# Kernel optimization log

Hardware: AMD Instinct MI355X
Metric: run time of the kernel (lower is better)

Reference implementation:

```python
import jax, jax.numpy as jnp
import numpy as np

B, S, D, H = 2, 2048, 1024, 16
DK = D // H


def setup_inputs() -> dict:
    key = jax.random.key(0)
    ks = jax.random.split(key, 11)
    scale = 1.0 / np.sqrt(D)
    inp = {
        "q": jax.random.normal(ks[0], (B, S, D), jnp.float32),
        "k": jax.random.normal(ks[1], (B, S, D), jnp.float32),
        "v": jax.random.normal(ks[2], (B, S, D), jnp.float32),
        # causal mask, broadcastable to (B, H, S, S); 0 = masked
        "mask": jnp.tril(jnp.ones((S, S), jnp.int32))[None, None, :, :],
        "wq": jax.random.normal(ks[3], (D, D), jnp.float32) * scale,
        "bq": jax.random.normal(ks[4], (D,), jnp.float32) * scale,
        "wk": jax.random.normal(ks[5], (D, D), jnp.float32) * scale,
        "bk": jax.random.normal(ks[6], (D,), jnp.float32) * scale,
        "wv": jax.random.normal(ks[7], (D, D), jnp.float32) * scale,
        "bv": jax.random.normal(ks[8], (D,), jnp.float32) * scale,
        "wo": jax.random.normal(ks[9], (D, D), jnp.float32) * scale,
        "bo": jax.random.normal(ks[10], (D,), jnp.float32) * scale,
    }
    return inp


def reference(q, k, v, mask, wq, bq, wk, bk, wv, bv, wo, bo):
    # Linear projections (torch Linear: y = x @ W^T + b)
    Q = jnp.einsum('bsd,ed->bse', q, wq) + bq
    K = jnp.einsum('bsd,ed->bse', k, wk) + bk
    V = jnp.einsum('bsd,ed->bse', v, wv) + bv
    # split heads -> (B, H, S, d_k)
    Q = Q.reshape(B, S, H, DK).transpose(0, 2, 1, 3)
    K = K.reshape(B, S, H, DK).transpose(0, 2, 1, 3)
    V = V.reshape(B, S, H, DK).transpose(0, 2, 1, 3)
    # naive full-score attention, faithful to the source
    scores = jnp.einsum('bhqd,bhkd->bhqk', Q, K) / jnp.sqrt(jnp.float32(DK))
    scores = jnp.where(mask == 0, -jnp.inf, scores)
    attn = jax.nn.softmax(scores, axis=-1)
    out = jnp.einsum('bhqk,bhkd->bhqd', attn, V)
    # merge heads -> (B, S, D)
    out = out.transpose(0, 2, 1, 3).reshape(B, S, D)
    return jnp.einsum('bsd,ed->bse', out, wo) + bo
```

## Files before the change

kernel.cpp:

```cpp
#include <hip/hip_runtime.h>
#include <hip/hip_bf16.h>
#include <cstdint>

constexpr int Bc = 2, Sc = 2048, Dc = 1024, Hc = 16;
constexpr int Mtok = Bc * Sc;

typedef __bf16 bf16;
typedef __bf16 bf16x8 __attribute__((ext_vector_type(8)));
typedef float  f32x4  __attribute__((ext_vector_type(4)));

__device__ __forceinline__ void gld_lds16(const bf16* g, bf16* l) {
  __builtin_amdgcn_global_load_lds(
      (__attribute__((address_space(1))) void*)(void*)g,
      (__attribute__((address_space(3))) void*)l, 16, 0, 0);
}

__global__ __launch_bounds__(256) void convert_all(
    const float* __restrict__ q, const float* __restrict__ k,
    const float* __restrict__ v, const float* __restrict__ wq,
    const float* __restrict__ wk, const float* __restrict__ wv,
    const float* __restrict__ wo, bf16* __restrict__ ws)
{
  constexpr size_t NQ = (size_t)Mtok * Dc;
  constexpr size_t NW = (size_t)Dc * Dc;
  const size_t e = ((size_t)blockIdx.x * 256 + threadIdx.x) * 8;
  const float* src; bf16* dst;
  if (e < 3 * NQ) {
    src = (e < NQ) ? q + e : (e < 2 * NQ) ? k + (e - NQ) : v + (e - 2 * NQ);
    dst = ws + e;
  } else {
    const size_t w = e - 3 * NQ;
    const float* wsrc = (w < NW) ? wq : (w < 2 * NW) ? wk : (w < 3 * NW) ? wv : wo;
    src = wsrc + (w & (NW - 1));
    dst = ws + 5 * NQ + w;
  }
  f32x4 a = ((const f32x4*)src)[0];
  f32x4 b = ((const f32x4*)src)[1];
  bf16x8 t;
  t[0]=(bf16)a[0]; t[1]=(bf16)a[1]; t[2]=(bf16)a[2]; t[3]=(bf16)a[3];
  t[4]=(bf16)b[0]; t[5]=(bf16)b[1]; t[6]=(bf16)b[2]; t[7]=(bf16)b[3];
  *(bf16x8*)dst = t;
}

__global__ __launch_bounds__(256) void gemm_qkv(
    const bf16* __restrict__ Aq, const bf16* __restrict__ Ak,
    const bf16* __restrict__ Av, const bf16* __restrict__ Wb,
    const float* __restrict__ bq, const float* __restrict__ bk,
    const float* __restrict__ bv,
    bf16* __restrict__ Yq, bf16* __restrict__ Yk, bf16* __restrict__ Yv)
{
  __shared__ __attribute__((aligned(16))) bf16 As[128 * 32];
  __shared__ __attribute__((aligned(16))) bf16 Bs[128 * 32];

  const int z = blockIdx.z;
  const bf16*  A    = (z == 0) ? Aq : (z == 1) ? Ak : Av;
  const bf16*  Wz   = Wb + (size_t)z * Dc * Dc;
  const float* bias = (z == 0) ? bq : (z == 1) ? bk : bv;
  bf16*        Y    = (z == 0) ? Yq : (z == 1) ? Yk : Yv;

  const int m0 = blockIdx.x * 128, n0 = blockIdx.y * 128;
  const int tid = threadIdx.x, wave = tid >> 6, lane = tid & 63;
  const int quad = lane >> 4, l16 = lane & 15;
  const int rw = wave >> 1, cw = wave & 1;
  const int srow = wave * 16 + (lane >> 2);
  const int scol = (lane & 3) * 8;

  f32x4 acc[4][4] = {};

  for (int k0 = 0; k0 < Dc; k0 += 32) {
#pragma unroll
    for (int s = 0; s < 2; ++s) {
      const int row = s * 64 + srow;
      gld_lds16(A  + (size_t)(m0 + row) * Dc + k0 + scol, &As[s * 2048 + wave * 512]);
      gld_lds16(Wz + (size_t)(n0 + row) * Dc + k0 + scol, &Bs[s * 2048 + wave * 512]);
    }
    __syncthreads();
    bf16x8 af[4];
#pragma unroll
    for (int rt = 0; rt < 4; ++rt)
      af[rt] = *(const bf16x8*)&As[(rw * 64 + rt * 16 + l16) * 32 + quad * 8];
#pragma unroll
    for (int ct = 0; ct < 4; ++ct) {
      bf16x8 bfr = *(const bf16x8*)&Bs[(cw * 64 + ct * 16 + l16) * 32 + quad * 8];
#pragma unroll
      for (int rt = 0; rt < 4; ++rt)
        acc[rt][ct] = __builtin_amdgcn_mfma_f32_16x16x32_bf16(af[rt], bfr, acc[rt][ct], 0, 0, 0);
    }
    __syncthreads();
  }

#pragma unroll
  for (int ct = 0; ct < 4; ++ct) {
    const int col = n0 + cw * 64 + ct * 16 + l16;
    const float bvv = bias[col];
#pragma unroll
    for (int rt = 0; rt < 4; ++rt)
#pragma unroll
      for (int i = 0; i < 4; ++i) {
        const int row = m0 + rw * 64 + rt * 16 + quad * 4 + i;
        Y[(size_t)row * Dc + col] = (bf16)(acc[rt][ct][i] + bvv);
      }
  }
}

__global__ __launch_bounds__(256) void gemm_o(
    const bf16* __restrict__ A, const bf16* __restrict__ Wz,
    const float* __restrict__ bias, float* __restrict__ Y)
{
  __shared__ __attribute__((aligned(16))) bf16 As[64 * 32];
  __shared__ __attribute__((aligned(16))) bf16 Bs[128 * 32];

  const int m0 = blockIdx.x * 64, n0 = blockIdx.y * 128;
  const int tid = threadIdx.x, wave = tid >> 6, lane = tid & 63;
  const int quad = lane >> 4, l16 = lane & 15;
  const int srow = wave * 16 + (lane >> 2);
  const int scol = (lane & 3) * 8;

  f32x4 acc[4][2] = {};

  for (int k0 = 0; k0 < Dc; k0 += 32) {
    gld_lds16(A + (size_t)(m0 + srow) * Dc + k0 + scol, &As[wave * 512]);
#pragma unroll
    for (int s = 0; s < 2; ++s) {
      const int row = s * 64 + srow;
      gld_lds16(Wz + (size_t)(n0 + row) * Dc + k0 + scol, &Bs[s * 2048 + wave * 512]);
    }
    __syncthreads();
    bf16x8 af[4];
#pragma unroll
    for (int rt = 0; rt < 4; ++rt)
      af[rt] = *(const bf16x8*)&As[(rt * 16 + l16) * 32 + quad * 8];
#pragma unroll
    for (int ct = 0; ct < 2; ++ct) {
      bf16x8 bfr = *(const bf16x8*)&Bs[(wave * 32 + ct * 16 + l16) * 32 + quad * 8];
#pragma unroll
      for (int rt = 0; rt < 4; ++rt)
        acc[rt][ct] = __builtin_amdgcn_mfma_f32_16x16x32_bf16(af[rt], bfr, acc[rt][ct], 0, 0, 0);
    }
    __syncthreads();
  }

#pragma unroll
  for (int ct = 0; ct < 2; ++ct) {
    const int col = n0 + wave * 32 + ct * 16 + l16;
    const float bvv = bias[col];
#pragma unroll
    for (int rt = 0; rt < 4; ++rt)
#pragma unroll
      for (int i = 0; i < 4; ++i) {
        const int row = m0 + rt * 16 + quad * 4 + i;
        Y[(size_t)row * Dc + col] = acc[rt][ct][i] + bvv;
      }
  }
}

template <bool AF32, bool BF32, bool OUTF32>
__global__ __launch_bounds__(256) void gemm128(
    const void* __restrict__ Av, const void* __restrict__ Bv,
    const float* __restrict__ bias, void* __restrict__ Yv,
    int M, int N, int K)
{
  __shared__ __attribute__((aligned(16))) bf16 As[2][128][40];
  __shared__ __attribute__((aligned(16))) bf16 Bs[2][128][40];

  const int m0 = blockIdx.x * 128, n0 = blockIdx.y * 128;
  const int tid = threadIdx.x, wave = tid >> 6, lane = tid & 63;
  const int quad = lane >> 4, l16 = lane & 15;
  const int rw = wave >> 1, cw = wave & 1;
  const int srow = tid >> 1, sc = (tid & 1) * 16;

  f32x4 acc[4][4] = {};

  auto load = [&](const void* P, bool f32, int r0, int k0, bf16x8& lo, bf16x8& hi) {
    if (f32) {
      const float* s = (const float*)P + (size_t)(r0 + srow) * K + k0 + sc;
      f32x4 a0 = ((const f32x4*)s)[0], a1 = ((const f32x4*)s)[1];
      f32x4 a2 = ((const f32x4*)s)[2], a3 = ((const f32x4*)s)[3];
      lo[0]=(bf16)a0[0]; lo[1]=(bf16)a0[1]; lo[2]=(bf16)a0[2]; lo[3]=(bf16)a0[3];
      lo[4]=(bf16)a1[0]; lo[5]=(bf16)a1[1]; lo[6]=(bf16)a1[2]; lo[7]=(bf16)a1[3];
      hi[0]=(bf16)a2[0]; hi[1]=(bf16)a2[1]; hi[2]=(bf16)a2[2]; hi[3]=(bf16)a2[3];
      hi[4]=(bf16)a3[0]; hi[5]=(bf16)a3[1]; hi[6]=(bf16)a3[2]; hi[7]=(bf16)a3[3];
    } else {
      const bf16* s = (const bf16*)P + (size_t)(r0 + srow) * K + k0 + sc;
      lo = ((const bf16x8*)s)[0]; hi = ((const bf16x8*)s)[1];
    }
  };

  bf16x8 alo, ahi, blo, bhi;
  load(Av, AF32, m0, 0, alo, ahi); load(Bv, BF32, n0, 0, blo, bhi);
  *(bf16x8*)&As[0][srow][sc] = alo; *(bf16x8*)&As[0][srow][sc + 8] = ahi;
  *(bf16x8*)&Bs[0][srow][sc] = blo; *(bf16x8*)&Bs[0][srow][sc + 8] = bhi;

  const int NIT = K >> 5;
  for (int it = 0; it < NIT; ++it) {
    __syncthreads();
    const int cur = it & 1;
    const bool pf = (it + 1) < NIT;
    if (pf) { load(Av, AF32, m0, (it+1)*32, alo, ahi); load(Bv, BF32, n0, (it+1)*32, blo, bhi); }

    bf16x8 af[4];
#pragma unroll
    for (int rt = 0; rt < 4; ++rt)
      af[rt] = *(const bf16x8*)&As[cur][rw * 64 + rt * 16 + l16][quad * 8];
#pragma unroll
    for (int ct = 0; ct < 4; ++ct) {
      bf16x8 bfr = *(const bf16x8*)&Bs[cur][cw * 64 + ct * 16 + l16][quad * 8];
#pragma unroll
      for (int rt = 0; rt < 4; ++rt)
        acc[rt][ct] = __builtin_amdgcn_mfma_f32_16x16x32_bf16(af[rt], bfr, acc[rt][ct], 0, 0, 0);
    }
    if (pf) {
      const int nxt = cur ^ 1;
      *(bf16x8*)&As[nxt][srow][sc] = alo; *(bf16x8*)&As[nxt][srow][sc + 8] = ahi;
      *(bf16x8*)&Bs[nxt][srow][sc] = blo; *(bf16x8*)&Bs[nxt][srow][sc + 8] = bhi;
    }
  }

#pragma unroll
  for (int ct = 0; ct < 4; ++ct) {
    const int col = n0 + cw * 64 + ct * 16 + l16;
    const float bvv = bias[col];
#pragma unroll
    for (int rt = 0; rt < 4; ++rt)
#pragma unroll
      for (int i = 0; i < 4; ++i) {
        const int row = m0 + rw * 64 + rt * 16 + quad * 4 + i;
        const float vv = acc[rt][ct][i] + bvv;
        if constexpr (OUTF32) ((float*)Yv)[(size_t)row * N + col] = vv;
        else                  ((bf16*)Yv)[(size_t)row * N + col] = (bf16)vv;
      }
  }
}

__global__ __launch_bounds__(256) void transpose_v(
    const bf16* __restrict__ in, bf16* __restrict__ out)
{
  __shared__ __attribute__((aligned(16))) bf16 tile[64][72];
  const int s0 = blockIdx.x * 64, d0 = blockIdx.y * 64, b = blockIdx.z;
  const int t = threadIdx.x, r = t >> 2, c = (t & 3) * 16;

  const bf16* src = in + (size_t)(b * Sc + s0 + r) * Dc + d0 + c;
  *(bf16x8*)&tile[r][c]     = ((const bf16x8*)src)[0];
  *(bf16x8*)&tile[r][c + 8] = ((const bf16x8*)src)[1];
  __syncthreads();

  bf16x8 t0, t1;
#pragma unroll
  for (int j = 0; j < 8; ++j) t0[j] = tile[c + j][r];
#pragma unroll
  for (int j = 0; j < 8; ++j) t1[j] = tile[c + 8 + j][r];
  bf16* dst = out + (size_t)(b * Dc + d0 + r) * Sc + s0 + c;
  ((bf16x8*)dst)[0] = t0;
  ((bf16x8*)dst)[1] = t1;
}

__global__ __launch_bounds__(512) void attn3(
    const bf16* __restrict__ Q, const bf16* __restrict__ K,
    const bf16* __restrict__ Vt, bf16* __restrict__ O)
{
  __shared__ __attribute__((aligned(16))) bf16 Ks[2][64][68];
  __shared__ __attribute__((aligned(16))) bf16 Vs[2][64][68];
  __shared__ __attribute__((aligned(16))) bf16 Ps[8][16][68];

  const int bh = blockIdx.x, b = bh >> 4, h = bh & 15;
  const int pr = blockIdx.y;
  const int tid = threadIdx.x, wave = tid >> 6, lane = tid & 63;
  const int quad = lane >> 4, l16 = lane & 15;
  const int sr = tid >> 3, sc8 = (tid & 7) * 8;

  const bf16 onec = (bf16)1.0f;
  const bf16x8 ones = {onec, onec, onec, onec, onec, onec, onec, onec};

  for (int half = 0; half < 2; ++half) {
    const int qt = half ? (15 - pr) : pr;
    const int q0 = qt * 128;
    const int nkb = 2 * (qt + 1);

    const bf16* qrow = Q + (size_t)(b * Sc + q0 + wave * 16 + l16) * Dc + h * 64 + quad * 8;
    const bf16x8 aq0 = *(const bf16x8*)qrow;
    const bf16x8 aq1 = *(const bf16x8*)(qrow + 32);

    f32x4 oacc[4] = {{0,0,0,0},{0,0,0,0},{0,0,0,0},{0,0,0,0}};
    f32x4 lacc = {0, 0, 0, 0};

    __syncthreads();
    *(bf16x8*)&Ks[0][sr][sc8] = *(const bf16x8*)(K  + (size_t)(b * Sc + sr) * Dc + h * 64 + sc8);
    *(bf16x8*)&Vs[0][sr][sc8] = *(const bf16x8*)(Vt + (size_t)(b * Dc + h * 64 + sr) * Sc + sc8);

    for (int kb = 0; kb < nkb; ++kb) {
      __syncthreads();
      const int cur = kb & 1;
      const bool pf = (kb + 1) < nkb;
      bf16x8 kp, vp;
      if (pf) {
        kp = *(const bf16x8*)(K  + (size_t)(b * Sc + (kb + 1) * 64 + sr) * Dc + h * 64 + sc8);
        vp = *(const bf16x8*)(Vt + (size_t)(b * Dc + h * 64 + sr) * Sc + (kb + 1) * 64 + sc8);
      }

      f32x4 s[4] = {{0,0,0,0},{0,0,0,0},{0,0,0,0},{0,0,0,0}};
#pragma unroll
      for (int d2 = 0; d2 < 2; ++d2) {
        const bf16x8 a = d2 ? aq1 : aq0;
#pragma unroll
        for (int ct = 0; ct < 4; ++ct) {
          bf16x8 bk = *(const bf16x8*)&Ks[cur][ct * 16 + l16][d2 * 32 + quad * 8];
          s[ct] = __builtin_amdgcn_mfma_f32_16x16x32_bf16(a, bk, s[ct], 0, 0, 0);
        }
      }

      if (kb >= nkb - 2) {
        const int row = q0 + wave * 16 + quad * 4;
#pragma unroll
        for (int ct = 0; ct < 4; ++ct) {
          const int col = kb * 64 + ct * 16 + l16;
#pragma unroll
          for (int i = 0; i < 4; ++i) {
            const float e = (col > row + i) ? 0.f : __expf(s[ct][i] * 0.125f);
            Ps[wave][quad * 4 + i][ct * 16 + l16] = (bf16)e;
          }
        }
      } else {
#pragma unroll
        for (int ct = 0; ct < 4; ++ct)
#pragma unroll
          for (int i = 0; i < 4; ++i)
            Ps[wave][quad * 4 + i][ct * 16 + l16] = (bf16)__expf(s[ct][i] * 0.125f);
      }

      const bf16x8 ap0 = *(const bf16x8*)&Ps[wave][l16][quad * 8];
      const bf16x8 ap1 = *(const bf16x8*)&Ps[wave][l16][32 + quad * 8];

      lacc = __builtin_amdgcn_mfma_f32_16x16x32_bf16(ap0, ones, lacc, 0, 0, 0);
      lacc = __builtin_amdgcn_mfma_f32_16x16x32_bf16(ap1, ones, lacc, 0, 0, 0);

#pragma unroll
      for (int d2 = 0; d2 < 2; ++d2) {
        const bf16x8 ap = d2 ? ap1 : ap0;
#pragma unroll
        for (int ct = 0; ct < 4; ++ct) {
          bf16x8 bv = *(const bf16x8*)&Vs[cur][ct * 16 + l16][d2 * 32 + quad * 8];
          oacc[ct] = __builtin_amdgcn_mfma_f32_16x16x32_bf16(ap, bv, oacc[ct], 0, 0, 0);
        }
      }

      if (pf) {
        const int nxt = cur ^ 1;
        *(bf16x8*)&Ks[nxt][sr][sc8] = kp;
        *(bf16x8*)&Vs[nxt][sr][sc8] = vp;
      }
    }

    f32x4 rl;
#pragma unroll
    for (int i = 0; i < 4; ++i) rl[i] = 1.0f / lacc[i];
#pragma unroll
    for (int ct = 0; ct < 4; ++ct)
#pragma unroll
      for (int i = 0; i < 4; ++i)
        O[(size_t)(b * Sc + q0 + wave * 16 + quad * 4 + i) * Dc + h * 64 + ct * 16 + l16] =
            (bf16)(oacc[ct][i] * rl[i]);
  }
}

extern "C" void kernel_launch(void* const* d_in, const int* in_sizes, int n_in,
                              void* d_out, int out_size, void* d_ws, size_t ws_size,
                              hipStream_t stream)
{
  const float* q  = (const float*)d_in[0];
  const float* k  = (const float*)d_in[1];
  const float* v  = (const float*)d_in[2];
  const float* wq = (const float*)d_in[4];
  const float* bq = (const float*)d_in[5];
  const float* wk = (const float*)d_in[6];
  const float* bk = (const float*)d_in[7];
  const float* wv = (const float*)d_in[8];
  const float* bv = (const float*)d_in[9];
  const float* wo = (const float*)d_in[10];
  const float* bo = (const float*)d_in[11];
  float* out = (float*)d_out;

  constexpr size_t NQ = (size_t)Mtok * Dc;
  constexpr size_t NW = (size_t)Dc * Dc;
  bf16* W = (bf16*)d_ws;
  const dim3 ga(Hc * Bc, 8);
  const dim3 gt(Sc / 64, Dc / 64, Bc);

  const bool fancy = ws_size >= (size_t)(5 * NQ + 4 * NW) * 2;
  if (fancy) {
    bf16* xq = W;
    bf16* xk = W + NQ;
    bf16* xv = W + 2 * NQ;
    bf16* Qp = W + 3 * NQ;
    bf16* Kp = W + 4 * NQ;
    bf16* wb = W + 5 * NQ;
    bf16* Vp = W;
    bf16* AO = W + NQ;
    bf16* Vt = W + 2 * NQ;

    convert_all<<<8192, 256, 0, stream>>>(q, k, v, wq, wk, wv, wo, W);
    gemm_qkv<<<dim3(Mtok / 128, Dc / 128, 3), 256, 0, stream>>>(
        xq, xk, xv, wb, bq, bk, bv, Qp, Kp, Vp);
    transpose_v<<<gt, 256, 0, stream>>>(Vp, Vt);
    attn3<<<ga, 512, 0, stream>>>(Qp, Kp, Vt, AO);
    gemm_o<<<dim3(Mtok / 64, Dc / 128), 256, 0, stream>>>(AO, wb + 3 * NW, bo, out);
  } else {
    bf16* Qp = W;
    bf16* Kp = W + NQ;
    bf16* Vp = W + 2 * NQ;
    bf16* Vt = W + 3 * NQ;
    bf16* AO = W + 4 * NQ;
    const dim3 gg(Mtok / 128, Dc / 128);
    gemm128<true, true, false><<<gg, 256, 0, stream>>>(q, wq, bq, Qp, Mtok, Dc, Dc);
    gemm128<true, true, false><<<gg, 256, 0, stream>>>(k, wk, bk, Kp, Mtok, Dc, Dc);
    gemm128<true, true, false><<<gg, 256, 0, stream>>>(v, wv, bv, Vp, Mtok, Dc, Dc);
    transpose_v<<<gt, 256, 0, stream>>>(Vp, Vt);
    attn3<<<ga, 512, 0, stream>>>(Qp, Kp, Vt, AO);
    gemm128<false, true, true><<<gg, 256, 0, stream>>>(AO, wo, bo, out, Mtok, Dc, Dc);
  }
}
```

Measured before the change: 236.5 us.

## Fuse V transpose into QKV GEMM, deepen GEMM K-tile, retile attention blocks

```diff
diff --git a/kernel.cpp b/kernel.cpp
--- a/kernel.cpp
+++ b/kernel.cpp
@@ -6,6 +6,7 @@
 constexpr int Mtok = Bc * Sc;
 
 typedef __bf16 bf16;
+typedef __bf16 bf16x4 __attribute__((ext_vector_type(4)));
 typedef __bf16 bf16x8 __attribute__((ext_vector_type(8)));
 typedef float  f32x4  __attribute__((ext_vector_type(4)));
 
@@ -47,59 +48,81 @@
     const bf16* __restrict__ Av, const bf16* __restrict__ Wb,
     const float* __restrict__ bq, const float* __restrict__ bk,
     const float* __restrict__ bv,
-    bf16* __restrict__ Yq, bf16* __restrict__ Yk, bf16* __restrict__ Yv)
-{
-  __shared__ __attribute__((aligned(16))) bf16 As[128 * 32];
-  __shared__ __attribute__((aligned(16))) bf16 Bs[128 * 32];
+    bf16* __restrict__ Yq, bf16* __restrict__ Yk, bf16* __restrict__ Vt)
+{
+  __shared__ __attribute__((aligned(16))) bf16 As[128 * 64];
+  __shared__ __attribute__((aligned(16))) bf16 Bs[128 * 64];
 
   const int z = blockIdx.z;
   const bf16*  A    = (z == 0) ? Aq : (z == 1) ? Ak : Av;
   const bf16*  Wz   = Wb + (size_t)z * Dc * Dc;
   const float* bias = (z == 0) ? bq : (z == 1) ? bk : bv;
-  bf16*        Y    = (z == 0) ? Yq : (z == 1) ? Yk : Yv;
 
   const int m0 = blockIdx.x * 128, n0 = blockIdx.y * 128;
   const int tid = threadIdx.x, wave = tid >> 6, lane = tid & 63;
   const int quad = lane >> 4, l16 = lane & 15;
   const int rw = wave >> 1, cw = wave & 1;
-  const int srow = wave * 16 + (lane >> 2);
-  const int scol = (lane & 3) * 8;
+  const int srow = wave * 8 + (lane >> 3);
+  const int scol = (lane & 7) * 8;
 
   f32x4 acc[4][4] = {};
 
-  for (int k0 = 0; k0 < Dc; k0 += 32) {
-#pragma unroll
-    for (int s = 0; s < 2; ++s) {
-      const int row = s * 64 + srow;
-      gld_lds16(A  + (size_t)(m0 + row) * Dc + k0 + scol, &As[s * 2048 + wave * 512]);
-      gld_lds16(Wz + (size_t)(n0 + row) * Dc + k0 + scol, &Bs[s * 2048 + wave * 512]);
-    }
-    __syncthreads();
-    bf16x8 af[4];
-#pragma unroll
-    for (int rt = 0; rt < 4; ++rt)
-      af[rt] = *(const bf16x8*)&As[(rw * 64 + rt * 16 + l16) * 32 + quad * 8];
+  for (int k0 = 0; k0 < Dc; k0 += 64) {
+#pragma unroll
+    for (int s = 0; s < 4; ++s) {
+      const int row = s * 32 + srow;
+      bf16* base = &As[s * 2048 + wave * 512];
+      gld_lds16(A  + (size_t)(m0 + row) * Dc + k0 + scol, base);
+      bf16* baseB = &Bs[s * 2048 + wave * 512];
+      gld_lds16(Wz + (size_t)(n0 + row) * Dc + k0 + scol, baseB);
+    }
+    __syncthreads();
+#pragma unroll
+    for (int ks = 0; ks < 2; ++ks) {
+      bf16x8 af[4];
+#pragma unroll
+      for (int rt = 0; rt < 4; ++rt)
+        af[rt] = *(const bf16x8*)&As[(rw * 64 + rt * 16 + l16) * 64 + ks * 32 + quad * 8];
+#pragma unroll
+      for (int ct = 0; ct < 4; ++ct) {
+        bf16x8 bfr = *(const bf16x8*)&Bs[(cw * 64 + ct * 16 + l16) * 64 + ks * 32 + quad * 8];
+#pragma unroll
+        for (int rt = 0; rt < 4; ++rt)
+          acc[rt][ct] = __builtin_amdgcn_mfma_f32_16x16x32_bf16(af[rt], bfr, acc[rt][ct], 0, 0, 0);
+      }
+    }
+    __syncthreads();
+  }
+
+  if (z < 2) {
+    bf16* Y = (z == 0) ? Yq : Yk;
 #pragma unroll
     for (int ct = 0; ct < 4; ++ct) {
-      bf16x8 bfr = *(const bf16x8*)&Bs[(cw * 64 + ct * 16 + l16) * 32 + quad * 8];
+      const int col = n0 + cw * 64 + ct * 16 + l16;
+      const float bvv = bias[col];
 #pragma unroll
       for (int rt = 0; rt < 4; ++rt)
-        acc[rt][ct] = __builtin_amdgcn_mfma_f32_16x16x32_bf16(af[rt], bfr, acc[rt][ct], 0, 0, 0);
-    }
-    __syncthreads();
-  }
-
-#pragma unroll
-  for (int ct = 0; ct < 4; ++ct) {
-    const int col = n0 + cw * 64 + ct * 16 + l16;
-    const float bvv = bias[col];
-#pragma unroll
-    for (int rt = 0; rt < 4; ++rt)
-#pragma unroll
-      for (int i = 0; i < 4; ++i) {
-        const int row = m0 + rw * 64 + rt * 16 + quad * 4 + i;
-        Y[(size_t)row * Dc + col] = (bf16)(acc[rt][ct][i] + bvv);
-      }
+#pragma unroll
+        for (int i = 0; i < 4; ++i) {
+          const int row = m0 + rw * 64 + rt * 16 + quad * 4 + i;
+          Y[(size_t)row * Dc + col] = (bf16)(acc[rt][ct][i] + bvv);
+        }
+    }
+  } else {
+#pragma unroll
+    for (int ct = 0; ct < 4; ++ct) {
+      const int col = n0 + cw * 64 + ct * 16 + l16;
+      const float bvv = bias[col];
+#pragma unroll
+      for (int rt = 0; rt < 4; ++rt) {
+        const int row0 = m0 + rw * 64 + rt * 16 + quad * 4;
+        const int bb = row0 >> 11, s0 = row0 & 2047;
+        bf16x4 pk;
+#pragma unroll
+        for (int i = 0; i < 4; ++i) pk[i] = (bf16)(acc[rt][ct][i] + bvv);
+        *(bf16x4*)&Vt[((size_t)bb * Dc + col) * Sc + s0] = pk;
+      }
+    }
   }
 }
 
@@ -107,35 +130,40 @@
     const bf16* __restrict__ A, const bf16* __restrict__ Wz,
     const float* __restrict__ bias, float* __restrict__ Y)
 {
-  __shared__ __attribute__((aligned(16))) bf16 As[64 * 32];
-  __shared__ __attribute__((aligned(16))) bf16 Bs[128 * 32];
+  __shared__ __attribute__((aligned(16))) bf16 As[64 * 64];
+  __shared__ __attribute__((aligned(16))) bf16 Bs[128 * 64];
 
   const int m0 = blockIdx.x * 64, n0 = blockIdx.y * 128;
   const int tid = threadIdx.x, wave = tid >> 6, lane = tid & 63;
   const int quad = lane >> 4, l16 = lane & 15;
-  const int srow = wave * 16 + (lane >> 2);
-  const int scol = (lane & 3) * 8;
+  const int srow = wave * 8 + (lane >> 3);
+  const int scol = (lane & 7) * 8;
 
   f32x4 acc[4][2] = {};
 
-  for (int k0 = 0; k0 < Dc; k0 += 32) {
-    gld_lds16(A + (size_t)(m0 + srow) * Dc + k0 + scol, &As[wave * 512]);
-#pragma unroll
-    for (int s = 0; s < 2; ++s) {
-      const int row = s * 64 + srow;
-      gld_lds16(Wz + (size_t)(n0 + row) * Dc + k0 + scol, &Bs[s * 2048 + wave * 512]);
-    }
-    __syncthreads();
-    bf16x8 af[4];
-#pragma unroll
-    for (int rt = 0; rt < 4; ++rt)
-      af[rt] = *(const bf16x8*)&As[(rt * 16 + l16) * 32 + quad * 8];
-#pragma unroll
-    for (int ct = 0; ct < 2; ++ct) {
-      bf16x8 bfr = *(const bf16x8*)&Bs[(wave * 32 + ct * 16 + l16) * 32 + quad * 8];
+  for (int k0 = 0; k0 < Dc; k0 += 64) {
+#pragma unroll
+    for (int s = 0; s < 2; ++s)
+      gld_lds16(A + (size_t)(m0 + s * 32 + srow) * Dc + k0 + scol,
+                &As[s * 2048 + wave * 512]);
+#pragma unroll
+    for (int s = 0; s < 4; ++s)
+      gld_lds16(Wz + (size_t)(n0 + s * 32 + srow) * Dc + k0 + scol,
+                &Bs[s * 2048 + wave * 512]);
+    __syncthreads();
+#pragma unroll
+    for (int ks = 0; ks < 2; ++ks) {
+      bf16x8 af[4];
 #pragma unroll
       for (int rt = 0; rt < 4; ++rt)
-        acc[rt][ct] = __builtin_amdgcn_mfma_f32_16x16x32_bf16(af[rt], bfr, acc[rt][ct], 0, 0, 0);
+        af[rt] = *(const bf16x8*)&As[(rt * 16 + l16) * 64 + ks * 32 + quad * 8];
+#pragma unroll
+      for (int ct = 0; ct < 2; ++ct) {
+        bf16x8 bfr = *(const bf16x8*)&Bs[(wave * 32 + ct * 16 + l16) * 64 + ks * 32 + quad * 8];
+#pragma unroll
+        for (int rt = 0; rt < 4; ++rt)
+          acc[rt][ct] = __builtin_amdgcn_mfma_f32_16x16x32_bf16(af[rt], bfr, acc[rt][ct], 0, 0, 0);
+      }
     }
     __syncthreads();
   }
@@ -254,112 +282,119 @@
   ((bf16x8*)dst)[1] = t1;
 }
 
-__global__ __launch_bounds__(512) void attn3(
+__global__ __launch_bounds__(256) void attn4(
     const bf16* __restrict__ Q, const bf16* __restrict__ K,
     const bf16* __restrict__ Vt, bf16* __restrict__ O)
 {
   __shared__ __attribute__((aligned(16))) bf16 Ks[2][64][68];
   __shared__ __attribute__((aligned(16))) bf16 Vs[2][64][68];
-  __shared__ __attribute__((aligned(16))) bf16 Ps[8][16][68];
+  __shared__ __attribute__((aligned(16))) bf16 Ps[4][16][68];
 
   const int bh = blockIdx.x, b = bh >> 4, h = bh & 15;
-  const int pr = blockIdx.y;
+  const int qy = blockIdx.y;
+  const int qt = (qy & 8) ? ((qy & 24) | (7 - (qy & 7))) : qy;
+  const int q0 = qt * 64;
+  const int nkb = qt + 1;
+
   const int tid = threadIdx.x, wave = tid >> 6, lane = tid & 63;
   const int quad = lane >> 4, l16 = lane & 15;
-  const int sr = tid >> 3, sc8 = (tid & 7) * 8;
+  const int sr = tid >> 2, sc4 = (tid & 3) * 16;
 
   const bf16 onec = (bf16)1.0f;
   const bf16x8 ones = {onec, onec, onec, onec, onec, onec, onec, onec};
 
-  for (int half = 0; half < 2; ++half) {
-    const int qt = half ? (15 - pr) : pr;
-    const int q0 = qt * 128;
-    const int nkb = 2 * (qt + 1);
-
-    const bf16* qrow = Q + (size_t)(b * Sc + q0 + wave * 16 + l16) * Dc + h * 64 + quad * 8;
-    const bf16x8 aq0 = *(const bf16x8*)qrow;
-    const bf16x8 aq1 = *(const bf16x8*)(qrow + 32);
-
-    f32x4 oacc[4] = {{0,0,0,0},{0,0,0,0},{0,0,0,0},{0,0,0,0}};
-    f32x4 lacc = {0, 0, 0, 0};
-
-    __syncthreads();
-    *(bf16x8*)&Ks[0][sr][sc8] = *(const bf16x8*)(K  + (size_t)(b * Sc + sr) * Dc + h * 64 + sc8);
-    *(bf16x8*)&Vs[0][sr][sc8] = *(const bf16x8*)(Vt + (size_t)(b * Dc + h * 64 + sr) * Sc + sc8);
-
-    for (int kb = 0; kb < nkb; ++kb) {
-      __syncthreads();
-      const int cur = kb & 1;
-      const bool pf = (kb + 1) < nkb;
-      bf16x8 kp, vp;
-      if (pf) {
-        kp = *(const bf16x8*)(K  + (size_t)(b * Sc + (kb + 1) * 64 + sr) * Dc + h * 64 + sc8);
-        vp = *(const bf16x8*)(Vt + (size_t)(b * Dc + h * 64 + sr) * Sc + (kb + 1) * 64 + sc8);
-      }
-
-      f32x4 s[4] = {{0,0,0,0},{0,0,0,0},{0,0,0,0},{0,0,0,0}};
-#pragma unroll
-      for (int d2 = 0; d2 < 2; ++d2) {
-        const bf16x8 a = d2 ? aq1 : aq0;
-#pragma unroll
-        for (int ct = 0; ct < 4; ++ct) {
-          bf16x8 bk = *(const bf16x8*)&Ks[cur][ct * 16 + l16][d2 * 32 + quad * 8];
-          s[ct] = __builtin_amdgcn_mfma_f32_16x16x32_bf16(a, bk, s[ct], 0, 0, 0);
-        }
-      }
-
-      if (kb >= nkb - 2) {
-        const int row = q0 + wave * 16 + quad * 4;
-#pragma unroll
-        for (int ct = 0; ct < 4; ++ct) {
-          const int col = kb * 64 + ct * 16 + l16;
-#pragma unroll
-          for (int i = 0; i < 4; ++i) {
-            const float e = (col > row + i) ? 0.f : __expf(s[ct][i] * 0.125f);
-            Ps[wave][quad * 4 + i][ct * 16 + l16] = (bf16)e;
-          }
-        }
-      } else {
-#pragma unroll
-        for (int ct = 0; ct < 4; ++ct)
-#pragma unroll
-          for (int i = 0; i < 4; ++i)
-            Ps[wave][quad * 4 + i][ct * 16 + l16] = (bf16)__expf(s[ct][i] * 0.125f);
-      }
-
-      const bf16x8 ap0 = *(const bf16x8*)&Ps[wave][l16][quad * 8];
-      const bf16x8 ap1 = *(const bf16x8*)&Ps[wave][l16][32 + quad * 8];
-
-      lacc = __builtin_amdgcn_mfma_f32_16x16x32_bf16(ap0, ones, lacc, 0, 0, 0);
-      lacc = __builtin_amdgcn_mfma_f32_16x16x32_bf16(ap1, ones, lacc, 0, 0, 0);
-
-#pragma unroll
-      for (int d2 = 0; d2 < 2; ++d2) {
-        const bf16x8 ap = d2 ? ap1 : ap0;
-#pragma unroll
-        for (int ct = 0; ct < 4; ++ct) {
-          bf16x8 bv = *(const bf16x8*)&Vs[cur][ct * 16 + l16][d2 * 32 + quad * 8];
-          oacc[ct] = __builtin_amdgcn_mfma_f32_16x16x32_bf16(ap, bv, oacc[ct], 0, 0, 0);
-        }
-      }
-
-      if (pf) {
-        const int nxt = cur ^ 1;
-        *(bf16x8*)&Ks[nxt][sr][sc8] = kp;
-        *(bf16x8*)&Vs[nxt][sr][sc8] = vp;
-      }
-    }
-
-    f32x4 rl;
-#pragma unroll
-    for (int i = 0; i < 4; ++i) rl[i] = 1.0f / lacc[i];
-#pragma unroll
-    for (int ct = 0; ct < 4; ++ct)
-#pragma unroll
-      for (int i = 0; i < 4; ++i)
-        O[(size_t)(b * Sc + q0 + wave * 16 + quad * 4 + i) * Dc + h * 64 + ct * 16 + l16] =
-            (bf16)(oacc[ct][i] * rl[i]);
-  }
+  const bf16* qrow = Q + (size_t)(b * Sc + q0 + wave * 16 + l16) * Dc + h * 64 + quad * 8;
+  const bf16x8 aq0 = *(const bf16x8*)qrow;
+  const bf16x8 aq1 = *(const bf16x8*)(qrow + 32);
+
+  f32x4 oacc[4] = {{0,0,0,0},{0,0,0,0},{0,0,0,0},{0,0,0,0}};
+  f32x4 lacc = {0, 0, 0, 0};
+
+  {
+    const bf16* ksrc = K + (size_t)(b * Sc + sr) * Dc + h * 64 + sc4;
+    ((bf16x8*)&Ks[0][sr][sc4])[0] = ((const bf16x8*)ksrc)[0];
+    ((bf16x8*)&Ks[0][sr][sc4])[1] = ((const bf16x8*)ksrc)[1];
+    const bf16* vsrc = Vt + (size_t)(b * Dc + h * 64 + sr) * Sc + sc4;
+    ((bf16x8*)&Vs[0][sr][sc4])[0] = ((const bf16x8*)vsrc)[0];
+    ((bf16x8*)&Vs[0][sr][sc4])[1] = ((const bf16x8*)vsrc)[1];
+  }
+
+  for (int kb = 0; kb < nkb; ++kb) {
+    __syncthreads();
+    const int cur = kb & 1;
+    const bool pf = (kb + 1) < nkb;
+    bf16x8 kp0, kp1, vp0, vp1;
+    if (pf) {
+      const bf16* ksrc = K + (size_t)(b * Sc + (kb + 1) * 64 + sr) * Dc + h * 64 + sc4;
+      kp0 = ((const bf16x8*)ksrc)[0]; kp1 = ((const bf16x8*)ksrc)[1];
+      const bf16* vsrc = Vt + (size_t)(b * Dc + h * 64 + sr) * Sc + (kb + 1) * 64 + sc4;
+      vp0 = ((const bf16x8*)vsrc)[0]; vp1 = ((const bf16x8*)vsrc)[1];
+    }
+
+    f32x4 s[4] = {{0,0,0,0},{0,0,0,0},{0,0,0,0},{0,0,0,0}};
+#pragma unroll
+    for (int d2 = 0; d2 < 2; ++d2) {
+      const bf16x8 bq = d2 ? aq1 : aq0;
+#pragma unroll
+      for (int ct = 0; ct < 4; ++ct) {
+        bf16x8 ak = *(const bf16x8*)&Ks[cur][ct * 16 + l16][d2 * 32 + quad * 8];
+        s[ct] = __builtin_amdgcn_mfma_f32_16x16x32_bf16(ak, bq, s[ct], 0, 0, 0);
+      }
+    }
+
+    if (kb == nkb - 1) {
+      const int qcol = wave * 16 + l16;
+#pragma unroll
+      for (int ct = 0; ct < 4; ++ct) {
+        const int key0 = ct * 16 + quad * 4;
+        bf16x4 pk;
+#pragma unroll
+        for (int i = 0; i < 4; ++i)
+          pk[i] = (bf16)((key0 + i > qcol) ? 0.f : __expf(s[ct][i] * 0.125f));
+        *(bf16x4*)&Ps[wave][l16][key0] = pk;
+      }
+    } else {
+#pragma unroll
+      for (int ct = 0; ct < 4; ++ct) {
+        bf16x4 pk;
+#pragma unroll
+        for (int i = 0; i < 4; ++i) pk[i] = (bf16)__expf(s[ct][i] * 0.125f);
+        *(bf16x4*)&Ps[wave][l16][ct * 16 + quad * 4] = pk;
+      }
+    }
+
+    const bf16x8 ap0 = *(const bf16x8*)&Ps[wave][l16][quad * 8];
+    const bf16x8 ap1 = *(const bf16x8*)&Ps[wave][l16][32 + quad * 8];
+
+    lacc = __builtin_amdgcn_mfma_f32_16x16x32_bf16(ap0, ones, lacc, 0, 0, 0);
+    lacc = __builtin_amdgcn_mfma_f32_16x16x32_bf16(ap1, ones, lacc, 0, 0, 0);
+
+#pragma unroll
+    for (int d2 = 0; d2 < 2; ++d2) {
+      const bf16x8 ap = d2 ? ap1 : ap0;
+#pragma unroll
+      for (int ct = 0; ct < 4; ++ct) {
+        bf16x8 bv = *(const bf16x8*)&Vs[cur][ct * 16 + l16][d2 * 32 + quad * 8];
+        oacc[ct] = __builtin_amdgcn_mfma_f32_16x16x32_bf16(ap, bv, oacc[ct], 0, 0, 0);
+      }
+    }
+
+    if (pf) {
+      const int nxt = cur ^ 1;
+      ((bf16x8*)&Ks[nxt][sr][sc4])[0] = kp0; ((bf16x8*)&Ks[nxt][sr][sc4])[1] = kp1;
+      ((bf16x8*)&Vs[nxt][sr][sc4])[0] = vp0; ((bf16x8*)&Vs[nxt][sr][sc4])[1] = vp1;
+    }
+  }
+
+  f32x4 rl;
+#pragma unroll
+  for (int i = 0; i < 4; ++i) rl[i] = 1.0f / lacc[i];
+#pragma unroll
+  for (int ct = 0; ct < 4; ++ct)
+#pragma unroll
+    for (int i = 0; i < 4; ++i)
+      O[(size_t)(b * Sc + q0 + wave * 16 + quad * 4 + i) * Dc + h * 64 + ct * 16 + l16] =
+          (bf16)(oacc[ct][i] * rl[i]);
 }
 
 extern "C" void kernel_launch(void* const* d_in, const int* in_sizes, int n_in,
@@ -382,10 +417,10 @@
   constexpr size_t NQ = (size_t)Mtok * Dc;
   constexpr size_t NW = (size_t)Dc * Dc;
   bf16* W = (bf16*)d_ws;
-  const dim3 ga(Hc * Bc, 8);
+  const dim3 ga(Hc * Bc, 32);
   const dim3 gt(Sc / 64, Dc / 64, Bc);
 
-  const bool fancy = ws_size >= (size_t)(5 * NQ + 4 * NW) * 2;
+  const bool fancy = ws_size >= (size_t)(6 * NQ + 4 * NW) * 2;
   if (fancy) {
     bf16* xq = W;
     bf16* xk = W + NQ;
@@ -393,15 +428,13 @@
     bf16* Qp = W + 3 * NQ;
     bf16* Kp = W + 4 * NQ;
     bf16* wb = W + 5 * NQ;
-    bf16* Vp = W;
-    bf16* AO = W + NQ;
-    bf16* Vt = W + 2 * NQ;
+    bf16* Vt = W + 5 * NQ + 4 * NW;
+    bf16* AO = W;
 
     convert_all<<<8192, 256, 0, stream>>>(q, k, v, wq, wk, wv, wo, W);
     gemm_qkv<<<dim3(Mtok / 128, Dc / 128, 3), 256, 0, stream>>>(
-        xq, xk, xv, wb, bq, bk, bv, Qp, Kp, Vp);
-    transpose_v<<<gt, 256, 0, stream>>>(Vp, Vt);
-    attn3<<<ga, 512, 0, stream>>>(Qp, Kp, Vt, AO);
+        xq, xk, xv, wb, bq, bk, bv, Qp, Kp, Vt);
+    attn4<<<ga, 256, 0, stream>>>(Qp, Kp, Vt, AO);
     gemm_o<<<dim3(Mtok / 64, Dc / 128), 256, 0, stream>>>(AO, wb + 3 * NW, bo, out);
   } else {
     bf16* Qp = W;
@@ -414,7 +447,7 @@
     gemm128<true, true, false><<<gg, 256, 0, stream>>>(k, wk, bk, Kp, Mtok, Dc, Dc);
     gemm128<true, true, false><<<gg, 256, 0, stream>>>(v, wv, bv, Vp, Mtok, Dc, Dc);
     transpose_v<<<gt, 256, 0, stream>>>(Vp, Vt);
-    attn3<<<ga, 512, 0, stream>>>(Qp, Kp, Vt, AO);
+    attn4<<<ga, 256, 0, stream>>>(Qp, Kp, Vt, AO);
     gemm128<false, true, true><<<gg, 256, 0, stream>>>(AO, wo, bo, out, Mtok, Dc, Dc);
   }
 }
```

Result: no change. 240.5 us (+1.7%).
